# Kernel tuning notes

Hardware: AMD Instinct MI355X
Metric: run time of the kernel (lower is better)

The kernel has to match this reference:

```python
import jax, jax.numpy as jnp
import numpy as np

N_AGENTS = 32
STATE_DIM = 512
EMBED = 64
BATCH = 32768


def setup_inputs() -> dict:
    key = jax.random.key(0)
    ks = jax.random.split(key, 16)
    g = lambda k, shape, fan_in: jax.random.normal(k, shape, jnp.float32) / np.sqrt(fan_in)
    return {
        "agent_qs": jax.random.normal(ks[0], (BATCH, N_AGENTS), jnp.float32),
        "states": jax.random.normal(ks[1], (BATCH, STATE_DIM), jnp.float32),
        # hyper_w1: Linear(state,E) -> ReLU -> Linear(E, n_agents*E)
        "w1_l1_w": g(ks[2], (EMBED, STATE_DIM), STATE_DIM),
        "w1_l1_b": jnp.zeros((EMBED,), jnp.float32),
        "w1_l2_w": g(ks[3], (N_AGENTS * EMBED, EMBED), EMBED),
        "w1_l2_b": jnp.zeros((N_AGENTS * EMBED,), jnp.float32),
        # hyper_w2: Linear(state,E) -> ReLU -> Linear(E, E)
        "w2_l1_w": g(ks[4], (EMBED, STATE_DIM), STATE_DIM),
        "w2_l1_b": jnp.zeros((EMBED,), jnp.float32),
        "w2_l2_w": g(ks[5], (EMBED, EMBED), EMBED),
        "w2_l2_b": jnp.zeros((EMBED,), jnp.float32),
        # hyper_b1: Linear(state, E)
        "b1_w": g(ks[6], (EMBED, STATE_DIM), STATE_DIM),
        "b1_b": jnp.zeros((EMBED,), jnp.float32),
        # hyper_b2: Linear(state,E) -> ReLU -> Linear(E, 1)
        "b2_l1_w": g(ks[7], (EMBED, STATE_DIM), STATE_DIM),
        "b2_l1_b": jnp.zeros((EMBED,), jnp.float32),
        "b2_l2_w": g(ks[8], (1, EMBED), EMBED),
        "b2_l2_b": jnp.zeros((1,), jnp.float32),
    }


def _linear(x, w, b):
    return x @ w.T + b


def reference(agent_qs, states,
              w1_l1_w, w1_l1_b, w1_l2_w, w1_l2_b,
              w2_l1_w, w2_l1_b, w2_l2_w, w2_l2_b,
              b1_w, b1_b, b2_l1_w, b2_l1_b, b2_l2_w, b2_l2_b):
    B = agent_qs.shape[0]
    # hypernetworks producing per-sample weights
    w1 = jnp.abs(_linear(jax.nn.relu(_linear(states, w1_l1_w, w1_l1_b)), w1_l2_w, w1_l2_b))
    w1 = w1.reshape(B, N_AGENTS, EMBED)                      # [B, A, E]
    b1 = _linear(states, b1_w, b1_b)                         # [B, E]
    hidden = jax.nn.elu(jnp.einsum('ba,bae->be', agent_qs, w1) + b1)  # [B, E]
    w2 = jnp.abs(_linear(jax.nn.relu(_linear(states, w2_l1_w, w2_l1_b)), w2_l2_w, w2_l2_b))  # [B, E]
    b2 = _linear(jax.nn.relu(_linear(states, b2_l1_w, b2_l1_b)), b2_l2_w, b2_l2_b)           # [B, 1]
    q_total = jnp.einsum('be,be->b', hidden, w2) + b2[:, 0]  # [B]
    return q_total
```

## Files before the change

kernel.cpp:

```cpp
#include <hip/hip_runtime.h>

typedef unsigned short u16;
typedef unsigned int u32;
typedef short bf16x8 __attribute__((ext_vector_type(8)));
typedef float f32x4 __attribute__((ext_vector_type(4)));
typedef u16 u16x4 __attribute__((ext_vector_type(4)));

#define NAG 32
#define STATE 512
#define EMBED 64
#define TB 64

#define OFF_W1L1 0
#define OFF_W2L1 32768
#define OFF_B1W  65536
#define OFF_B2L1 98304
#define OFF_W1L2 131072
#define OFF_W2L2 262144
#define WS_TOTAL 266240

#define Y_STR    200
#define SB_OFF   12800
#define SB_STR   72
#define SB_BUF   (64 * 72)
#define W1BS_OFF 22016
#define QST_OFF  24064
#define QST_STR  68
#define PBUF_OFF 12800
#define PBUF_STR 68
#define PBUF_WV  (64 * 68)
#define QACC_OFF  30208
#define QACC2_OFF 30336
#define B2WV_OFF  30464
#define SMEM_U16  30592

__device__ __forceinline__ float bf2f(u16 u) {
    u32 i = ((u32)u) << 16; float f;
    __builtin_memcpy(&f, &i, 4); return f;
}
__device__ __forceinline__ u16 f2bf(float f) {
    u32 i; __builtin_memcpy(&i, &f, 4);
    return (u16)((i + 0x8000u) >> 16);
}
__device__ __forceinline__ bf16x8 ld8(const u16* p) {
    return *reinterpret_cast<const bf16x8*>(p);
}
__device__ __forceinline__ bf16x8 cvt8(f32x4 a, f32x4 b) {
    bf16x8 r;
#pragma unroll
    for (int i = 0; i < 4; ++i) r[i]     = (short)f2bf(a[i]);
#pragma unroll
    for (int i = 0; i < 4; ++i) r[i + 4] = (short)f2bf(b[i]);
    return r;
}

__global__ __launch_bounds__(256) void cvt_weights(
    const float* __restrict__ w1l1w, const float* __restrict__ w2l1w,
    const float* __restrict__ b1w,   const float* __restrict__ b2l1w,
    const float* __restrict__ w1l2w, const float* __restrict__ w2l2w,
    u16* __restrict__ ws)
{
    int idx = blockIdx.x * 256 + threadIdx.x;
    const float* src; int off;
    if      (idx < OFF_W2L1)  { src = w1l1w; off = OFF_W1L1; }
    else if (idx < OFF_B1W)   { src = w2l1w; off = OFF_W2L1; }
    else if (idx < OFF_B2L1)  { src = b1w;   off = OFF_B1W;  }
    else if (idx < OFF_W1L2)  { src = b2l1w; off = OFF_B2L1; }
    else if (idx < OFF_W2L2)  { src = w1l2w; off = OFF_W1L2; }
    else if (idx < WS_TOTAL)  { src = w2l2w; off = OFF_W2L2; }
    else return;
    ws[idx] = f2bf(src[idx - off]);
}

__global__ __launch_bounds__(256, 2) void qmix_kernel(
    const float* __restrict__ qs,    const float* __restrict__ st,
    const u16*  __restrict__ wsb,
    const float* __restrict__ w1l1b, const float* __restrict__ w1l2b,
    const float* __restrict__ w2l1b, const float* __restrict__ w2l2b,
    const float* __restrict__ b1b,   const float* __restrict__ b2l1b,
    const float* __restrict__ b2l2w, const float* __restrict__ b2l2b,
    float* __restrict__ out)
{
    __shared__ u16 smem[SMEM_U16];
    float* qaccF  = (float*)(smem + QACC_OFF);
    float* qacc2F = (float*)(smem + QACC2_OFF);
    float* b2wvF  = (float*)(smem + B2WV_OFF);

    const int t    = threadIdx.x;
    const int wave = t >> 6, lane = t & 63;
    const int m = lane & 15, quad = lane >> 4;
    const int sbase = blockIdx.x * TB;

    if (t < 64) b2wvF[t] = b2l2w[t];
    {
        const float* qp = qs + (size_t)sbase * NAG + t * 8;
        f32x4 q0 = *reinterpret_cast<const f32x4*>(qp);
        f32x4 q1 = *reinterpret_cast<const f32x4*>(qp + 4);
        const int s = t >> 2, a0 = (t & 3) * 8;
#pragma unroll
        for (int j = 0; j < 4; ++j) smem[QST_OFF + (a0 + j) * QST_STR + s]     = f2bf(q0[j]);
#pragma unroll
        for (int j = 0; j < 4; ++j) smem[QST_OFF + (a0 + 4 + j) * QST_STR + s] = f2bf(q1[j]);
        f32x4 w0 = *reinterpret_cast<const f32x4*>(w1l2b + t * 8);
        f32x4 w1 = *reinterpret_cast<const f32x4*>(w1l2b + t * 8 + 4);
        *reinterpret_cast<bf16x8*>(&smem[W1BS_OFF + t * 8]) = cvt8(w0, w1);
    }

    const int ss1 = t >> 3, c8 = t & 7;
    const float* stb = st + (size_t)sbase * STATE;

    {
        const float* g1 = stb + (size_t)ss1 * STATE + c8 * 8;
        const float* g2 = g1 + (size_t)32 * STATE;
        f32x4 a0 = *reinterpret_cast<const f32x4*>(g1);
        f32x4 a1 = *reinterpret_cast<const f32x4*>(g1 + 4);
        f32x4 a2 = *reinterpret_cast<const f32x4*>(g2);
        f32x4 a3 = *reinterpret_cast<const f32x4*>(g2 + 4);
        u16* dst = smem + SB_OFF;
        *reinterpret_cast<bf16x8*>(&dst[ss1 * SB_STR + c8 * 8])        = cvt8(a0, a1);
        *reinterpret_cast<bf16x8*>(&dst[(ss1 + 32) * SB_STR + c8 * 8]) = cvt8(a2, a3);
    }

    const u16* wAw = wsb + (size_t)(wave * 64) * STATE;
    bf16x8 bfr[2][4][2];
#pragma unroll
    for (int ot = 0; ot < 4; ++ot) {
        const u16* wr = wAw + (size_t)(ot * 16 + m) * STATE + quad * 8;
        bfr[0][ot][0] = ld8(wr);
        bfr[0][ot][1] = ld8(wr + 32);
    }
    __syncthreads();

    f32x4 acc[4][4] = {};
#pragma unroll
    for (int ks = 0; ks < 8; ++ks) {
        f32x4 sa0 = {}, sa1 = {}, sa2 = {}, sa3 = {};
        if (ks < 7) {
            const float* g1 = stb + (size_t)ss1 * STATE + (ks + 1) * 64 + c8 * 8;
            const float* g2 = g1 + (size_t)32 * STATE;
            sa0 = *reinterpret_cast<const f32x4*>(g1);
            sa1 = *reinterpret_cast<const f32x4*>(g1 + 4);
            sa2 = *reinterpret_cast<const f32x4*>(g2);
            sa3 = *reinterpret_cast<const f32x4*>(g2 + 4);
#pragma unroll
            for (int ot = 0; ot < 4; ++ot) {
                const u16* wr = wAw + (size_t)(ot * 16 + m) * STATE + (ks + 1) * 64 + quad * 8;
                bfr[(ks + 1) & 1][ot][0] = ld8(wr);
                bfr[(ks + 1) & 1][ot][1] = ld8(wr + 32);
            }
        }
        const u16* sbc = smem + SB_OFF + (ks & 1) * SB_BUF;
#pragma unroll
        for (int st2 = 0; st2 < 4; ++st2) {
            const int row = st2 * 16 + m;
            bf16x8 af0 = ld8(&sbc[row * SB_STR + quad * 8]);
            bf16x8 af1 = ld8(&sbc[row * SB_STR + (quad + 4) * 8]);
#pragma unroll
            for (int ot = 0; ot < 4; ++ot)
                acc[st2][ot] = __builtin_amdgcn_mfma_f32_16x16x32_bf16(af0, bfr[ks & 1][ot][0], acc[st2][ot], 0, 0, 0);
#pragma unroll
            for (int ot = 0; ot < 4; ++ot)
                acc[st2][ot] = __builtin_amdgcn_mfma_f32_16x16x32_bf16(af1, bfr[ks & 1][ot][1], acc[st2][ot], 0, 0, 0);
        }
        if (ks < 7) {
            u16* dst = smem + SB_OFF + ((ks + 1) & 1) * SB_BUF;
            *reinterpret_cast<bf16x8*>(&dst[ss1 * SB_STR + c8 * 8])        = cvt8(sa0, sa1);
            *reinterpret_cast<bf16x8*>(&dst[(ss1 + 32) * SB_STR + c8 * 8]) = cvt8(sa2, sa3);
        }
        __syncthreads();
    }

    if (wave != 3) {
        const float* barr = (wave == 0) ? w1l1b : (wave == 1) ? w2l1b : b1b;
        const bool isrelu = (wave != 2);
        float wb[4];
#pragma unroll
        for (int ot = 0; ot < 4; ++ot) wb[ot] = barr[ot * 16 + m];
#pragma unroll
        for (int st2 = 0; st2 < 4; ++st2)
#pragma unroll
            for (int ot = 0; ot < 4; ++ot)
#pragma unroll
                for (int r = 0; r < 4; ++r) {
                    float v = acc[st2][ot][r] + wb[ot];
                    if (isrelu) v = fmaxf(v, 0.f);
                    smem[(st2 * 16 + quad * 4 + r) * Y_STR + wave * 64 + ot * 16 + m] = f2bf(v);
                }
    } else {
        float wb[4], bw[4];
#pragma unroll
        for (int ot = 0; ot < 4; ++ot) wb[ot] = b2l1b[ot * 16 + m];
#pragma unroll
        for (int ot = 0; ot < 4; ++ot) bw[ot] = b2wvF[ot * 16 + m];
#pragma unroll
        for (int st2 = 0; st2 < 4; ++st2)
#pragma unroll
            for (int r = 0; r < 4; ++r) {
                float pd = 0.f;
#pragma unroll
                for (int ot = 0; ot < 4; ++ot)
                    pd += fmaxf(acc[st2][ot][r] + wb[ot], 0.f) * bw[ot];
#pragma unroll
                for (int off = 1; off < 16; off <<= 1) pd += __shfl_xor(pd, off, 64);
                if (m == 0) qacc2F[st2 * 16 + quad * 4 + r] = pd;
            }
    }
    __syncthreads();

    bf16x8 h1f[4][2];
#pragma unroll
    for (int st2 = 0; st2 < 4; ++st2) {
        h1f[st2][0] = ld8(&smem[(st2 * 16 + m) * Y_STR + quad * 8]);
        h1f[st2][1] = ld8(&smem[(st2 * 16 + m) * Y_STR + 32 + quad * 8]);
    }

    const u16* wB = wsb + OFF_W1L2 + (size_t)(wave * 8) * 64 * EMBED;
    bf16x8 bb[2][4][2];
#pragma unroll
    for (int ot = 0; ot < 4; ++ot) {
        const u16* wr = wB + (size_t)(ot * 16 + m) * EMBED + quad * 8;
        bb[0][ot][0] = ld8(wr);
        bb[0][ot][1] = ld8(wr + 32);
    }

    f32x4 hacc[4][4] = {};
#pragma unroll
    for (int ag = 0; ag < 8; ++ag) {
        if (ag < 7) {
#pragma unroll
            for (int ot = 0; ot < 4; ++ot) {
                const u16* wr = wB + (size_t)((ag + 1) * 64 + ot * 16 + m) * EMBED + quad * 8;
                bb[(ag + 1) & 1][ot][0] = ld8(wr);
                bb[(ag + 1) & 1][ot][1] = ld8(wr + 32);
            }
        }
        const int a = wave * 8 + ag;
        float bias[4];
#pragma unroll
        for (int ot = 0; ot < 4; ++ot) bias[ot] = bf2f(smem[W1BS_OFF + a * EMBED + ot * 16 + m]);
#pragma unroll
        for (int st2 = 0; st2 < 4; ++st2) {
            u16x4 qv = *reinterpret_cast<const u16x4*>(&smem[QST_OFF + a * QST_STR + st2 * 16 + quad * 4]);
#pragma unroll
            for (int ot = 0; ot < 4; ++ot) {
                f32x4 p = {};
                p = __builtin_amdgcn_mfma_f32_16x16x32_bf16(h1f[st2][0], bb[ag & 1][ot][0], p, 0, 0, 0);
                p = __builtin_amdgcn_mfma_f32_16x16x32_bf16(h1f[st2][1], bb[ag & 1][ot][1], p, 0, 0, 0);
#pragma unroll
                for (int r = 0; r < 4; ++r)
                    hacc[st2][ot][r] += bf2f((u16)qv[r]) * fabsf(p[r] + bias[ot]);
            }
        }
    }
    __syncthreads();

#pragma unroll
    for (int st2 = 0; st2 < 4; ++st2)
#pragma unroll
        for (int ot = 0; ot < 4; ++ot)
#pragma unroll
            for (int r = 0; r < 4; ++r)
                smem[PBUF_OFF + wave * PBUF_WV + (st2 * 16 + quad * 4 + r) * PBUF_STR + ot * 16 + m]
                    = f2bf(hacc[st2][ot][r]);
    __syncthreads();

    {
        const int s  = wave * 16 + (lane & 15);
        const int eb = (lane >> 4) * 16;
        float v[16];
#pragma unroll
        for (int j = 0; j < 16; ++j) v[j] = 0.f;
#pragma unroll
        for (int pw = 0; pw < 4; ++pw) {
#pragma unroll
            for (int c = 0; c < 4; ++c) {
                u16x4 x = *reinterpret_cast<const u16x4*>(
                    &smem[PBUF_OFF + pw * PBUF_WV + s * PBUF_STR + eb + c * 4]);
#pragma unroll
                for (int j = 0; j < 4; ++j) v[c * 4 + j] += bf2f((u16)x[j]);
            }
        }
        bf16x8 bv0 = ld8(&smem[s * Y_STR + 128 + eb]);
        bf16x8 bv1 = ld8(&smem[s * Y_STR + 128 + eb + 8]);
        bf16x8 o0, o1;
#pragma unroll
        for (int j = 0; j < 8; ++j) {
            float h0 = v[j] + bf2f((u16)bv0[j]);
            h0 = (h0 > 0.f) ? h0 : (__expf(h0) - 1.f);
            o0[j] = (short)f2bf(h0);
            float h1 = v[8 + j] + bf2f((u16)bv1[j]);
            h1 = (h1 > 0.f) ? h1 : (__expf(h1) - 1.f);
            o1[j] = (short)f2bf(h1);
        }
        *reinterpret_cast<bf16x8*>(&smem[s * Y_STR + 128 + eb])     = o0;
        *reinterpret_cast<bf16x8*>(&smem[s * Y_STR + 128 + eb + 8]) = o1;
    }
    __syncthreads();

    const int s0 = wave * 16;
    bf16x8 h2f0 = ld8(&smem[(s0 + m) * Y_STR + 64 + quad * 8]);
    bf16x8 h2f1 = ld8(&smem[(s0 + m) * Y_STR + 96 + quad * 8]);

    f32x4 qp = {};
#pragma unroll
    for (int tp = 0; tp < 4; ++tp) {
        const u16* wc = wsb + OFF_W2L2 + (size_t)(tp * 16 + m) * EMBED + quad * 8;
        bf16x8 c0 = ld8(wc);
        bf16x8 c1 = ld8(wc + 32);
        f32x4 p = {};
        p = __builtin_amdgcn_mfma_f32_16x16x32_bf16(h2f0, c0, p, 0, 0, 0);
        p = __builtin_amdgcn_mfma_f32_16x16x32_bf16(h2f1, c1, p, 0, 0, 0);
        const float bias = w2l2b[tp * 16 + m];
#pragma unroll
        for (int r = 0; r < 4; ++r)
            qp[r] += bf2f(smem[(s0 + quad * 4 + r) * Y_STR + 128 + tp * 16 + m]) * fabsf(p[r] + bias);
    }
#pragma unroll
    for (int off = 1; off < 16; off <<= 1) {
#pragma unroll
        for (int r = 0; r < 4; ++r) qp[r] += __shfl_xor(qp[r], off, 64);
    }
    if (m == 0) {
#pragma unroll
        for (int r = 0; r < 4; ++r) qaccF[s0 + quad * 4 + r] = qp[r];
    }
    __syncthreads();

    if (t < TB) out[sbase + t] = qaccF[t] + qacc2F[t] + b2l2b[0];
}

extern "C" void kernel_launch(void* const* d_in, const int* in_sizes, int n_in,
                              void* d_out, int out_size, void* d_ws, size_t ws_size,
                              hipStream_t stream)
{
    const float* qs    = (const float*)d_in[0];
    const float* st    = (const float*)d_in[1];
    const float* w1l1w = (const float*)d_in[2];
    const float* w1l1b = (const float*)d_in[3];
    const float* w1l2w = (const float*)d_in[4];
    const float* w1l2b = (const float*)d_in[5];
    const float* w2l1w = (const float*)d_in[6];
    const float* w2l1b = (const float*)d_in[7];
    const float* w2l2w = (const float*)d_in[8];
    const float* w2l2b = (const float*)d_in[9];
    const float* b1w   = (const float*)d_in[10];
    const float* b1b   = (const float*)d_in[11];
    const float* b2l1w = (const float*)d_in[12];
    const float* b2l1b = (const float*)d_in[13];
    const float* b2l2w = (const float*)d_in[14];
    const float* b2l2b = (const float*)d_in[15];

    u16* wsb = (u16*)d_ws;

    cvt_weights<<<(WS_TOTAL + 255) / 256, 256, 0, stream>>>(
        w1l1w, w2l1w, b1w, b2l1w, w1l2w, w2l2w, wsb);

    int B = in_sizes[0] / NAG;
    int grid = B / TB;
    qmix_kernel<<<grid, 256, 0, stream>>>(
        qs, st, wsb,
        w1l1b, w1l2b, w2l1b, w2l2b, b1b, b2l1b, b2l2w, b2l2b,
        (float*)d_out);
}
```

Before: 157.3 us.

## Double block to 512 threads and split per-wave work across eight waves

The block now has eight waves instead of four. Each wave takes 32 output columns of the first-layer GEMM, and for the w1 mixing stage the work is split by agent group and sample half. This spreads the same 64-sample tile over more waves, cutting per-thread accumulator registers and raising latency hiding. The launch bound asks for four blocks per CU. The reduction buffer stride is changed to 72, and the b2 partials are split into two halves. The risk is the extra syncthreads cost across 512 threads, half the waves idle in the final stage, and dropping the prefetch double-buffering of the w1l2 weights.

```diff
diff --git a/kernel.cpp b/kernel.cpp
--- a/kernel.cpp
+++ b/kernel.cpp
@@ -27,12 +27,12 @@
 #define QST_OFF  24064
 #define QST_STR  68
 #define PBUF_OFF 12800
-#define PBUF_STR 68
-#define PBUF_WV  (64 * 68)
-#define QACC_OFF  30208
-#define QACC2_OFF 30336
-#define B2WV_OFF  30464
-#define SMEM_U16  30592
+#define PBUF_STR 72
+#define PBUF_WV  (64 * 72)
+#define QACC_OFF  31232
+#define QACC2_OFF 31360
+#define B2WV_OFF  31616
+#define SMEM_U16  31744
 
 __device__ __forceinline__ float bf2f(u16 u) {
     u32 i = ((u32)u) << 16; float f;
@@ -72,7 +72,7 @@
     ws[idx] = f2bf(src[idx - off]);
 }
 
-__global__ __launch_bounds__(256, 2) void qmix_kernel(
+__global__ __launch_bounds__(512, 4) void qmix_kernel(
     const float* __restrict__ qs,    const float* __restrict__ st,
     const u16*  __restrict__ wsb,
     const float* __restrict__ w1l1b, const float* __restrict__ w1l2b,
@@ -92,7 +92,7 @@
     const int sbase = blockIdx.x * TB;
 
     if (t < 64) b2wvF[t] = b2l2w[t];
-    {
+    if (t < 256) {
         const float* qp = qs + (size_t)sbase * NAG + t * 8;
         f32x4 q0 = *reinterpret_cast<const f32x4*>(qp);
         f32x4 q1 = *reinterpret_cast<const f32x4*>(qp + 4);
@@ -101,49 +101,42 @@
         for (int j = 0; j < 4; ++j) smem[QST_OFF + (a0 + j) * QST_STR + s]     = f2bf(q0[j]);
 #pragma unroll
         for (int j = 0; j < 4; ++j) smem[QST_OFF + (a0 + 4 + j) * QST_STR + s] = f2bf(q1[j]);
-        f32x4 w0 = *reinterpret_cast<const f32x4*>(w1l2b + t * 8);
-        f32x4 w1 = *reinterpret_cast<const f32x4*>(w1l2b + t * 8 + 4);
-        *reinterpret_cast<bf16x8*>(&smem[W1BS_OFF + t * 8]) = cvt8(w0, w1);
+    } else {
+        const int i = t & 255;
+        f32x4 w0 = *reinterpret_cast<const f32x4*>(w1l2b + i * 8);
+        f32x4 w1 = *reinterpret_cast<const f32x4*>(w1l2b + i * 8 + 4);
+        *reinterpret_cast<bf16x8*>(&smem[W1BS_OFF + i * 8]) = cvt8(w0, w1);
     }
 
     const int ss1 = t >> 3, c8 = t & 7;
     const float* stb = st + (size_t)sbase * STATE;
-
     {
         const float* g1 = stb + (size_t)ss1 * STATE + c8 * 8;
-        const float* g2 = g1 + (size_t)32 * STATE;
         f32x4 a0 = *reinterpret_cast<const f32x4*>(g1);
         f32x4 a1 = *reinterpret_cast<const f32x4*>(g1 + 4);
-        f32x4 a2 = *reinterpret_cast<const f32x4*>(g2);
-        f32x4 a3 = *reinterpret_cast<const f32x4*>(g2 + 4);
-        u16* dst = smem + SB_OFF;
-        *reinterpret_cast<bf16x8*>(&dst[ss1 * SB_STR + c8 * 8])        = cvt8(a0, a1);
-        *reinterpret_cast<bf16x8*>(&dst[(ss1 + 32) * SB_STR + c8 * 8]) = cvt8(a2, a3);
-    }
-
-    const u16* wAw = wsb + (size_t)(wave * 64) * STATE;
-    bf16x8 bfr[2][4][2];
-#pragma unroll
-    for (int ot = 0; ot < 4; ++ot) {
+        *reinterpret_cast<bf16x8*>(&smem[SB_OFF + ss1 * SB_STR + c8 * 8]) = cvt8(a0, a1);
+    }
+
+    const u16* wAw = wsb + (size_t)(wave * 32) * STATE;
+    bf16x8 bfr[2][2][2];
+#pragma unroll
+    for (int ot = 0; ot < 2; ++ot) {
         const u16* wr = wAw + (size_t)(ot * 16 + m) * STATE + quad * 8;
         bfr[0][ot][0] = ld8(wr);
         bfr[0][ot][1] = ld8(wr + 32);
     }
     __syncthreads();
 
-    f32x4 acc[4][4] = {};
+    f32x4 acc[4][2] = {};
 #pragma unroll
     for (int ks = 0; ks < 8; ++ks) {
-        f32x4 sa0 = {}, sa1 = {}, sa2 = {}, sa3 = {};
+        f32x4 sa0 = {}, sa1 = {};
         if (ks < 7) {
             const float* g1 = stb + (size_t)ss1 * STATE + (ks + 1) * 64 + c8 * 8;
-            const float* g2 = g1 + (size_t)32 * STATE;
             sa0 = *reinterpret_cast<const f32x4*>(g1);
             sa1 = *reinterpret_cast<const f32x4*>(g1 + 4);
-            sa2 = *reinterpret_cast<const f32x4*>(g2);
-            sa3 = *reinterpret_cast<const f32x4*>(g2 + 4);
-#pragma unroll
-            for (int ot = 0; ot < 4; ++ot) {
+#pragma unroll
+            for (int ot = 0; ot < 2; ++ot) {
                 const u16* wr = wAw + (size_t)(ot * 16 + m) * STATE + (ks + 1) * 64 + quad * 8;
                 bfr[(ks + 1) & 1][ot][0] = ld8(wr);
                 bfr[(ks + 1) & 1][ot][1] = ld8(wr + 32);
@@ -156,96 +149,92 @@
             bf16x8 af0 = ld8(&sbc[row * SB_STR + quad * 8]);
             bf16x8 af1 = ld8(&sbc[row * SB_STR + (quad + 4) * 8]);
 #pragma unroll
-            for (int ot = 0; ot < 4; ++ot)
+            for (int ot = 0; ot < 2; ++ot)
                 acc[st2][ot] = __builtin_amdgcn_mfma_f32_16x16x32_bf16(af0, bfr[ks & 1][ot][0], acc[st2][ot], 0, 0, 0);
 #pragma unroll
-            for (int ot = 0; ot < 4; ++ot)
+            for (int ot = 0; ot < 2; ++ot)
                 acc[st2][ot] = __builtin_amdgcn_mfma_f32_16x16x32_bf16(af1, bfr[ks & 1][ot][1], acc[st2][ot], 0, 0, 0);
         }
         if (ks < 7) {
             u16* dst = smem + SB_OFF + ((ks + 1) & 1) * SB_BUF;
-            *reinterpret_cast<bf16x8*>(&dst[ss1 * SB_STR + c8 * 8])        = cvt8(sa0, sa1);
-            *reinterpret_cast<bf16x8*>(&dst[(ss1 + 32) * SB_STR + c8 * 8]) = cvt8(sa2, sa3);
+            *reinterpret_cast<bf16x8*>(&dst[ss1 * SB_STR + c8 * 8]) = cvt8(sa0, sa1);
         }
         __syncthreads();
     }
 
-    if (wave != 3) {
-        const float* barr = (wave == 0) ? w1l1b : (wave == 1) ? w2l1b : b1b;
-        const bool isrelu = (wave != 2);
-        float wb[4];
-#pragma unroll
-        for (int ot = 0; ot < 4; ++ot) wb[ot] = barr[ot * 16 + m];
-#pragma unroll
-        for (int st2 = 0; st2 < 4; ++st2)
-#pragma unroll
-            for (int ot = 0; ot < 4; ++ot)
+    {
+        const int grp = wave >> 1, half = wave & 1;
+        if (grp < 3) {
+            const float* barr = (grp == 0) ? w1l1b : (grp == 1) ? w2l1b : b1b;
+            const bool isrelu = (grp != 2);
+            float wb[2];
+#pragma unroll
+            for (int ot = 0; ot < 2; ++ot) wb[ot] = barr[half * 32 + ot * 16 + m];
+#pragma unroll
+            for (int st2 = 0; st2 < 4; ++st2)
+#pragma unroll
+                for (int ot = 0; ot < 2; ++ot)
+#pragma unroll
+                    for (int r = 0; r < 4; ++r) {
+                        float v = acc[st2][ot][r] + wb[ot];
+                        if (isrelu) v = fmaxf(v, 0.f);
+                        smem[(st2 * 16 + quad * 4 + r) * Y_STR + grp * 64 + half * 32 + ot * 16 + m] = f2bf(v);
+                    }
+        } else {
+            float wb[2], bw[2];
+#pragma unroll
+            for (int ot = 0; ot < 2; ++ot) wb[ot] = b2l1b[half * 32 + ot * 16 + m];
+#pragma unroll
+            for (int ot = 0; ot < 2; ++ot) bw[ot] = b2wvF[half * 32 + ot * 16 + m];
+#pragma unroll
+            for (int st2 = 0; st2 < 4; ++st2)
 #pragma unroll
                 for (int r = 0; r < 4; ++r) {
-                    float v = acc[st2][ot][r] + wb[ot];
-                    if (isrelu) v = fmaxf(v, 0.f);
-                    smem[(st2 * 16 + quad * 4 + r) * Y_STR + wave * 64 + ot * 16 + m] = f2bf(v);
+                    float pd = 0.f;
+#pragma unroll
+                    for (int ot = 0; ot < 2; ++ot)
+                        pd += fmaxf(acc[st2][ot][r] + wb[ot], 0.f) * bw[ot];
+#pragma unroll
+                    for (int off = 1; off < 16; off <<= 1) pd += __shfl_xor(pd, off, 64);
+                    if (m == 0) qacc2F[half * 64 + st2 * 16 + quad * 4 + r] = pd;
                 }
-    } else {
-        float wb[4], bw[4];
-#pragma unroll
-        for (int ot = 0; ot < 4; ++ot) wb[ot] = b2l1b[ot * 16 + m];
-#pragma unroll
-        for (int ot = 0; ot < 4; ++ot) bw[ot] = b2wvF[ot * 16 + m];
-#pragma unroll
-        for (int st2 = 0; st2 < 4; ++st2)
-#pragma unroll
-            for (int r = 0; r < 4; ++r) {
-                float pd = 0.f;
-#pragma unroll
-                for (int ot = 0; ot < 4; ++ot)
-                    pd += fmaxf(acc[st2][ot][r] + wb[ot], 0.f) * bw[ot];
-#pragma unroll
-                for (int off = 1; off < 16; off <<= 1) pd += __shfl_xor(pd, off, 64);
-                if (m == 0) qacc2F[st2 * 16 + quad * 4 + r] = pd;
-            }
-    }
-    __syncthreads();
-
-    bf16x8 h1f[4][2];
-#pragma unroll
-    for (int st2 = 0; st2 < 4; ++st2) {
-        h1f[st2][0] = ld8(&smem[(st2 * 16 + m) * Y_STR + quad * 8]);
-        h1f[st2][1] = ld8(&smem[(st2 * 16 + m) * Y_STR + 32 + quad * 8]);
-    }
-
-    const u16* wB = wsb + OFF_W1L2 + (size_t)(wave * 8) * 64 * EMBED;
-    bf16x8 bb[2][4][2];
-#pragma unroll
-    for (int ot = 0; ot < 4; ++ot) {
-        const u16* wr = wB + (size_t)(ot * 16 + m) * EMBED + quad * 8;
-        bb[0][ot][0] = ld8(wr);
-        bb[0][ot][1] = ld8(wr + 32);
-    }
-
-    f32x4 hacc[4][4] = {};
+        }
+    }
+    __syncthreads();
+
+    const int ah = wave & 3, sh = wave >> 2;
+    bf16x8 h1f[2][2];
+#pragma unroll
+    for (int st2 = 0; st2 < 2; ++st2) {
+        const int row = sh * 32 + st2 * 16 + m;
+        h1f[st2][0] = ld8(&smem[row * Y_STR + quad * 8]);
+        h1f[st2][1] = ld8(&smem[row * Y_STR + 32 + quad * 8]);
+    }
+
+    const u16* wB = wsb + OFF_W1L2 + (size_t)(ah * 8) * 64 * EMBED;
+    f32x4 hacc[2][4] = {};
 #pragma unroll
     for (int ag = 0; ag < 8; ++ag) {
-        if (ag < 7) {
-#pragma unroll
-            for (int ot = 0; ot < 4; ++ot) {
-                const u16* wr = wB + (size_t)((ag + 1) * 64 + ot * 16 + m) * EMBED + quad * 8;
-                bb[(ag + 1) & 1][ot][0] = ld8(wr);
-                bb[(ag + 1) & 1][ot][1] = ld8(wr + 32);
-            }
-        }
-        const int a = wave * 8 + ag;
+        const int a = ah * 8 + ag;
+        bf16x8 bb[4][2];
+#pragma unroll
+        for (int ot = 0; ot < 4; ++ot) {
+            const u16* wr = wB + (size_t)(ag * 64 + ot * 16 + m) * EMBED + quad * 8;
+            bb[ot][0] = ld8(wr);
+            bb[ot][1] = ld8(wr + 32);
+        }
         float bias[4];
 #pragma unroll
         for (int ot = 0; ot < 4; ++ot) bias[ot] = bf2f(smem[W1BS_OFF + a * EMBED + ot * 16 + m]);
 #pragma unroll
-        for (int st2 = 0; st2 < 4; ++st2) {
-            u16x4 qv = *reinterpret_cast<const u16x4*>(&smem[QST_OFF + a * QST_STR + st2 * 16 + quad * 4]);
+        for (int st2 = 0; st2 < 2; ++st2) {
+            u16x4 qv = *reinterpret_cast<const u16x4*>(
+                &smem[QST_OFF + a * QST_STR + sh * 32 + st2 * 16 + quad * 4]);
 #pragma unroll
             for (int ot = 0; ot < 4; ++ot) {
                 f32x4 p = {};
-                p = __builtin_amdgcn_mfma_f32_16x16x32_bf16(h1f[st2][0], bb[ag & 1][ot][0], p, 0, 0, 0);
-                p = __builtin_amdgcn_mfma_f32_16x16x32_bf16(h1f[st2][1], bb[ag & 1][ot][1], p, 0, 0, 0);
+                p = __builtin_amdgcn_mfma_f32_16x16x32_bf16(h1f[st2][0], bb[ot][0], p, 0, 0, 0);
+                p = __builtin_amdgcn_mfma_f32_16x16x32_bf16(h1f[st2][1], bb[ot][1], p, 0, 0, 0);
 #pragma unroll
                 for (int r = 0; r < 4; ++r)
                     hacc[st2][ot][r] += bf2f((u16)qv[r]) * fabsf(p[r] + bias[ot]);
@@ -255,78 +244,77 @@
     __syncthreads();
 
 #pragma unroll
-    for (int st2 = 0; st2 < 4; ++st2)
+    for (int st2 = 0; st2 < 2; ++st2)
 #pragma unroll
         for (int ot = 0; ot < 4; ++ot)
 #pragma unroll
             for (int r = 0; r < 4; ++r)
-                smem[PBUF_OFF + wave * PBUF_WV + (st2 * 16 + quad * 4 + r) * PBUF_STR + ot * 16 + m]
+                smem[PBUF_OFF + ah * PBUF_WV
+                     + (sh * 32 + st2 * 16 + quad * 4 + r) * PBUF_STR + ot * 16 + m]
                     = f2bf(hacc[st2][ot][r]);
     __syncthreads();
 
     {
-        const int s  = wave * 16 + (lane & 15);
-        const int eb = (lane >> 4) * 16;
-        float v[16];
-#pragma unroll
-        for (int j = 0; j < 16; ++j) v[j] = 0.f;
+        const int s  = t >> 3;
+        const int eb = (t & 7) * 8;
+        float v[8];
+#pragma unroll
+        for (int j = 0; j < 8; ++j) v[j] = 0.f;
 #pragma unroll
         for (int pw = 0; pw < 4; ++pw) {
-#pragma unroll
-            for (int c = 0; c < 4; ++c) {
-                u16x4 x = *reinterpret_cast<const u16x4*>(
-                    &smem[PBUF_OFF + pw * PBUF_WV + s * PBUF_STR + eb + c * 4]);
-#pragma unroll
-                for (int j = 0; j < 4; ++j) v[c * 4 + j] += bf2f((u16)x[j]);
-            }
-        }
-        bf16x8 bv0 = ld8(&smem[s * Y_STR + 128 + eb]);
-        bf16x8 bv1 = ld8(&smem[s * Y_STR + 128 + eb + 8]);
-        bf16x8 o0, o1;
+            u16x4 x0 = *reinterpret_cast<const u16x4*>(
+                &smem[PBUF_OFF + pw * PBUF_WV + s * PBUF_STR + eb]);
+            u16x4 x1 = *reinterpret_cast<const u16x4*>(
+                &smem[PBUF_OFF + pw * PBUF_WV + s * PBUF_STR + eb + 4]);
+#pragma unroll
+            for (int j = 0; j < 4; ++j) v[j]     += bf2f((u16)x0[j]);
+#pragma unroll
+            for (int j = 0; j < 4; ++j) v[4 + j] += bf2f((u16)x1[j]);
+        }
+        bf16x8 bv = ld8(&smem[s * Y_STR + 128 + eb]);
+        bf16x8 o;
 #pragma unroll
         for (int j = 0; j < 8; ++j) {
-            float h0 = v[j] + bf2f((u16)bv0[j]);
-            h0 = (h0 > 0.f) ? h0 : (__expf(h0) - 1.f);
-            o0[j] = (short)f2bf(h0);
-            float h1 = v[8 + j] + bf2f((u16)bv1[j]);
-            h1 = (h1 > 0.f) ? h1 : (__expf(h1) - 1.f);
-            o1[j] = (short)f2bf(h1);
-        }
-        *reinterpret_cast<bf16x8*>(&smem[s * Y_STR + 128 + eb])     = o0;
-        *reinterpret_cast<bf16x8*>(&smem[s * Y_STR + 128 + eb + 8]) = o1;
-    }
-    __syncthreads();
-
-    const int s0 = wave * 16;
-    bf16x8 h2f0 = ld8(&smem[(s0 + m) * Y_STR + 64 + quad * 8]);
-    bf16x8 h2f1 = ld8(&smem[(s0 + m) * Y_STR + 96 + quad * 8]);
-
-    f32x4 qp = {};
-#pragma unroll
-    for (int tp = 0; tp < 4; ++tp) {
-        const u16* wc = wsb + OFF_W2L2 + (size_t)(tp * 16 + m) * EMBED + quad * 8;
-        bf16x8 c0 = ld8(wc);
-        bf16x8 c1 = ld8(wc + 32);
-        f32x4 p = {};
-        p = __builtin_amdgcn_mfma_f32_16x16x32_bf16(h2f0, c0, p, 0, 0, 0);
-        p = __builtin_amdgcn_mfma_f32_16x16x32_bf16(h2f1, c1, p, 0, 0, 0);
-        const float bias = w2l2b[tp * 16 + m];
-#pragma unroll
-        for (int r = 0; r < 4; ++r)
-            qp[r] += bf2f(smem[(s0 + quad * 4 + r) * Y_STR + 128 + tp * 16 + m]) * fabsf(p[r] + bias);
-    }
-#pragma unroll
-    for (int off = 1; off < 16; off <<= 1) {
-#pragma unroll
-        for (int r = 0; r < 4; ++r) qp[r] += __shfl_xor(qp[r], off, 64);
-    }
-    if (m == 0) {
-#pragma unroll
-        for (int r = 0; r < 4; ++r) qaccF[s0 + quad * 4 + r] = qp[r];
-    }
-    __syncthreads();
-
-    if (t < TB) out[sbase + t] = qaccF[t] + qacc2F[t] + b2l2b[0];
+            float h = v[j] + bf2f((u16)bv[j]);
+            h = (h > 0.f) ? h : (__expf(h) - 1.f);
+            o[j] = (short)f2bf(h);
+        }
+        *reinterpret_cast<bf16x8*>(&smem[s * Y_STR + 128 + eb]) = o;
+    }
+    __syncthreads();
+
+    if (wave < 4) {
+        const int s0 = wave * 16;
+        bf16x8 h2f0 = ld8(&smem[(s0 + m) * Y_STR + 64 + quad * 8]);
+        bf16x8 h2f1 = ld8(&smem[(s0 + m) * Y_STR + 96 + quad * 8]);
+
+        f32x4 qp = {};
+#pragma unroll
+        for (int tp = 0; tp < 4; ++tp) {
+            const u16* wc = wsb + OFF_W2L2 + (size_t)(tp * 16 + m) * EMBED + quad * 8;
+            bf16x8 c0 = ld8(wc);
+            bf16x8 c1 = ld8(wc + 32);
+            f32x4 p = {};
+            p = __builtin_amdgcn_mfma_f32_16x16x32_bf16(h2f0, c0, p, 0, 0, 0);
+            p = __builtin_amdgcn_mfma_f32_16x16x32_bf16(h2f1, c1, p, 0, 0, 0);
+            const float bias = w2l2b[tp * 16 + m];
+#pragma unroll
+            for (int r = 0; r < 4; ++r)
+                qp[r] += bf2f(smem[(s0 + quad * 4 + r) * Y_STR + 128 + tp * 16 + m]) * fabsf(p[r] + bias);
+        }
+#pragma unroll
+        for (int off = 1; off < 16; off <<= 1) {
+#pragma unroll
+            for (int r = 0; r < 4; ++r) qp[r] += __shfl_xor(qp[r], off, 64);
+        }
+        if (m == 0) {
+#pragma unroll
+            for (int r = 0; r < 4; ++r) qaccF[s0 + quad * 4 + r] = qp[r];
+        }
+    }
+    __syncthreads();
+
+    if (t < TB) out[sbase + t] = qaccF[t] + qacc2F[t] + qacc2F[64 + t] + b2l2b[0];
 }
 
 extern "C" void kernel_launch(void* const* d_in, const int* in_sizes, int n_in,
@@ -357,7 +345,7 @@
 
     int B = in_sizes[0] / NAG;
     int grid = B / TB;
-    qmix_kernel<<<grid, 256, 0, stream>>>(
+    qmix_kernel<<<grid, 512, 0, stream>>>(
         qs, st, wsb,
         w1l1b, w1l2b, w2l1b, w2l2b, b1b, b2l1b, b2l2w, b2l2b,
         (float*)d_out);
```

Result: slower. 168.5 us (+7.2%).

## Stage weight tiles into LDS via global_load_lds DMA with XOR swizzle

Applied to the files above, without the earlier changes.

Replaces the per-lane register prefetch of the layer-1 and W1-layer-2 weight fragments with direct global-to-LDS DMA (global_load_lds) into an XOR-swizzled shared buffer. MFMA operands are then read from LDS. The double-buffered state staging and register prefetch pipeline are removed, so each k-step now does a load, a full waitcnt(0) and two barriers before compute. This lowers register pressure and VGPR traffic but serialises loads and compute, and it grows the LDS footprint, which may reduce occupancy.

```diff
diff --git a/kernel.cpp b/kernel.cpp
--- a/kernel.cpp
+++ b/kernel.cpp
@@ -19,20 +19,21 @@
 #define OFF_W2L2 262144
 #define WS_TOTAL 266240
 
+#define WBUF_OFF 0
+#define SB_OFF   16384
+#define SB_STR   72
+#define QST_OFF  20992
+#define QST_STR  68
+#define W1BS_OFF 23168
+#define Y_OFF    25216
 #define Y_STR    200
-#define SB_OFF   12800
-#define SB_STR   72
-#define SB_BUF   (64 * 72)
-#define W1BS_OFF 22016
-#define QST_OFF  24064
-#define QST_STR  68
-#define PBUF_OFF 12800
-#define PBUF_STR 68
-#define PBUF_WV  (64 * 68)
-#define QACC_OFF  30208
-#define QACC2_OFF 30336
-#define B2WV_OFF  30464
-#define SMEM_U16  30592
+#define PBUF_OFF 0
+#define PBUF_STR 72
+#define PBUF_WV  (64 * 72)
+#define QACC_OFF  38016
+#define QACC2_OFF 38144
+#define B2WV_OFF  38272
+#define SMEM_U16  38400
 
 __device__ __forceinline__ float bf2f(u16 u) {
     u32 i = ((u32)u) << 16; float f;
@@ -52,6 +53,11 @@
 #pragma unroll
     for (int i = 0; i < 4; ++i) r[i + 4] = (short)f2bf(b[i]);
     return r;
+}
+__device__ __forceinline__ void dma16(const void* g, void* l) {
+    __builtin_amdgcn_global_load_lds(
+        (const __attribute__((address_space(1))) u32*)g,
+        (__attribute__((address_space(3))) u32*)l, 16, 0, 0);
 }
 
 __global__ __launch_bounds__(256) void cvt_weights(
@@ -89,6 +95,8 @@
     const int t    = threadIdx.x;
     const int wave = t >> 6, lane = t & 63;
     const int m = lane & 15, quad = lane >> 4;
+    const int rsub = lane >> 3, cch = lane & 7;
+    const int sc = cch ^ rsub;
     const int sbase = blockIdx.x * TB;
 
     if (t < 64) b2wvF[t] = b2l2w[t];
@@ -109,68 +117,47 @@
     const int ss1 = t >> 3, c8 = t & 7;
     const float* stb = st + (size_t)sbase * STATE;
 
-    {
-        const float* g1 = stb + (size_t)ss1 * STATE + c8 * 8;
-        const float* g2 = g1 + (size_t)32 * STATE;
-        f32x4 a0 = *reinterpret_cast<const f32x4*>(g1);
-        f32x4 a1 = *reinterpret_cast<const f32x4*>(g1 + 4);
-        f32x4 a2 = *reinterpret_cast<const f32x4*>(g2);
-        f32x4 a3 = *reinterpret_cast<const f32x4*>(g2 + 4);
-        u16* dst = smem + SB_OFF;
-        *reinterpret_cast<bf16x8*>(&dst[ss1 * SB_STR + c8 * 8])        = cvt8(a0, a1);
-        *reinterpret_cast<bf16x8*>(&dst[(ss1 + 32) * SB_STR + c8 * 8]) = cvt8(a2, a3);
-    }
-
-    const u16* wAw = wsb + (size_t)(wave * 64) * STATE;
-    bf16x8 bfr[2][4][2];
-#pragma unroll
-    for (int ot = 0; ot < 4; ++ot) {
-        const u16* wr = wAw + (size_t)(ot * 16 + m) * STATE + quad * 8;
-        bfr[0][ot][0] = ld8(wr);
-        bfr[0][ot][1] = ld8(wr + 32);
-    }
-    __syncthreads();
-
     f32x4 acc[4][4] = {};
-#pragma unroll
     for (int ks = 0; ks < 8; ++ks) {
-        f32x4 sa0 = {}, sa1 = {}, sa2 = {}, sa3 = {};
-        if (ks < 7) {
-            const float* g1 = stb + (size_t)ss1 * STATE + (ks + 1) * 64 + c8 * 8;
+        __syncthreads();
+#pragma unroll
+        for (int j = 0; j < 8; ++j)
+            dma16(wsb + (size_t)(wave * 64 + j * 8 + rsub) * STATE + ks * 64 + sc * 8,
+                  &smem[WBUF_OFF + (wave * 64 + j * 8) * 64]);
+        {
+            const float* g1 = stb + (size_t)ss1 * STATE + ks * 64 + c8 * 8;
             const float* g2 = g1 + (size_t)32 * STATE;
-            sa0 = *reinterpret_cast<const f32x4*>(g1);
-            sa1 = *reinterpret_cast<const f32x4*>(g1 + 4);
-            sa2 = *reinterpret_cast<const f32x4*>(g2);
-            sa3 = *reinterpret_cast<const f32x4*>(g2 + 4);
-#pragma unroll
-            for (int ot = 0; ot < 4; ++ot) {
-                const u16* wr = wAw + (size_t)(ot * 16 + m) * STATE + (ks + 1) * 64 + quad * 8;
-                bfr[(ks + 1) & 1][ot][0] = ld8(wr);
-                bfr[(ks + 1) & 1][ot][1] = ld8(wr + 32);
-            }
-        }
-        const u16* sbc = smem + SB_OFF + (ks & 1) * SB_BUF;
+            f32x4 a0 = *reinterpret_cast<const f32x4*>(g1);
+            f32x4 a1 = *reinterpret_cast<const f32x4*>(g1 + 4);
+            f32x4 a2 = *reinterpret_cast<const f32x4*>(g2);
+            f32x4 a3 = *reinterpret_cast<const f32x4*>(g2 + 4);
+            *reinterpret_cast<bf16x8*>(&smem[SB_OFF + ss1 * SB_STR + c8 * 8])        = cvt8(a0, a1);
+            *reinterpret_cast<bf16x8*>(&smem[SB_OFF + (ss1 + 32) * SB_STR + c8 * 8]) = cvt8(a2, a3);
+        }
+        __builtin_amdgcn_s_waitcnt(0);
+        __syncthreads();
+        bf16x8 wfr[4][2];
+#pragma unroll
+        for (int ot = 0; ot < 4; ++ot) {
+            const int brow = wave * 64 + ot * 16 + m;
+            wfr[ot][0] = ld8(&smem[WBUF_OFF + brow * 64 + ((quad ^ (brow & 7))) * 8]);
+            wfr[ot][1] = ld8(&smem[WBUF_OFF + brow * 64 + (((quad + 4) ^ (brow & 7))) * 8]);
+        }
 #pragma unroll
         for (int st2 = 0; st2 < 4; ++st2) {
             const int row = st2 * 16 + m;
-            bf16x8 af0 = ld8(&sbc[row * SB_STR + quad * 8]);
-            bf16x8 af1 = ld8(&sbc[row * SB_STR + (quad + 4) * 8]);
+            bf16x8 af0 = ld8(&smem[SB_OFF + row * SB_STR + quad * 8]);
+            bf16x8 af1 = ld8(&smem[SB_OFF + row * SB_STR + (quad + 4) * 8]);
 #pragma unroll
             for (int ot = 0; ot < 4; ++ot)
-                acc[st2][ot] = __builtin_amdgcn_mfma_f32_16x16x32_bf16(af0, bfr[ks & 1][ot][0], acc[st2][ot], 0, 0, 0);
+                acc[st2][ot] = __builtin_amdgcn_mfma_f32_16x16x32_bf16(af0, wfr[ot][0], acc[st2][ot], 0, 0, 0);
 #pragma unroll
             for (int ot = 0; ot < 4; ++ot)
-                acc[st2][ot] = __builtin_amdgcn_mfma_f32_16x16x32_bf16(af1, bfr[ks & 1][ot][1], acc[st2][ot], 0, 0, 0);
-        }
-        if (ks < 7) {
-            u16* dst = smem + SB_OFF + ((ks + 1) & 1) * SB_BUF;
-            *reinterpret_cast<bf16x8*>(&dst[ss1 * SB_STR + c8 * 8])        = cvt8(sa0, sa1);
-            *reinterpret_cast<bf16x8*>(&dst[(ss1 + 32) * SB_STR + c8 * 8]) = cvt8(sa2, sa3);
-        }
-        __syncthreads();
-    }
-
-    if (wave != 3) {
+                acc[st2][ot] = __builtin_amdgcn_mfma_f32_16x16x32_bf16(af1, wfr[ot][1], acc[st2][ot], 0, 0, 0);
+        }
+    }
+
+    if (wave < 3) {
         const float* barr = (wave == 0) ? w1l1b : (wave == 1) ? w2l1b : b1b;
         const bool isrelu = (wave != 2);
         float wb[4];
@@ -184,7 +171,7 @@
                 for (int r = 0; r < 4; ++r) {
                     float v = acc[st2][ot][r] + wb[ot];
                     if (isrelu) v = fmaxf(v, 0.f);
-                    smem[(st2 * 16 + quad * 4 + r) * Y_STR + wave * 64 + ot * 16 + m] = f2bf(v);
+                    smem[Y_OFF + (st2 * 16 + quad * 4 + r) * Y_STR + wave * 64 + ot * 16 + m] = f2bf(v);
                 }
     } else {
         float wb[4], bw[4];
@@ -210,58 +197,56 @@
     bf16x8 h1f[4][2];
 #pragma unroll
     for (int st2 = 0; st2 < 4; ++st2) {
-        h1f[st2][0] = ld8(&smem[(st2 * 16 + m) * Y_STR + quad * 8]);
-        h1f[st2][1] = ld8(&smem[(st2 * 16 + m) * Y_STR + 32 + quad * 8]);
-    }
-
-    const u16* wB = wsb + OFF_W1L2 + (size_t)(wave * 8) * 64 * EMBED;
-    bf16x8 bb[2][4][2];
-#pragma unroll
-    for (int ot = 0; ot < 4; ++ot) {
-        const u16* wr = wB + (size_t)(ot * 16 + m) * EMBED + quad * 8;
-        bb[0][ot][0] = ld8(wr);
-        bb[0][ot][1] = ld8(wr + 32);
+        h1f[st2][0] = ld8(&smem[Y_OFF + (st2 * 16 + m) * Y_STR + quad * 8]);
+        h1f[st2][1] = ld8(&smem[Y_OFF + (st2 * 16 + m) * Y_STR + 32 + quad * 8]);
     }
 
     f32x4 hacc[4][4] = {};
-#pragma unroll
-    for (int ag = 0; ag < 8; ++ag) {
-        if (ag < 7) {
-#pragma unroll
-            for (int ot = 0; ot < 4; ++ot) {
-                const u16* wr = wB + (size_t)((ag + 1) * 64 + ot * 16 + m) * EMBED + quad * 8;
-                bb[(ag + 1) & 1][ot][0] = ld8(wr);
-                bb[(ag + 1) & 1][ot][1] = ld8(wr + 32);
+    for (int j = 0; j < 8; ++j) {
+        __syncthreads();
+        const int a = wave * 8 + j;
+#pragma unroll
+        for (int jj = 0; jj < 8; ++jj)
+            dma16(wsb + OFF_W1L2 + (size_t)(a * 64 + jj * 8 + rsub) * EMBED + sc * 8,
+                  &smem[WBUF_OFF + (wave * 64 + jj * 8) * 64]);
+        __builtin_amdgcn_s_waitcnt(0);
+        __syncthreads();
+        bf16x8 wf[4][2];
+#pragma unroll
+        for (int tp = 0; tp < 4; ++tp) {
+            const int brow = wave * 64 + tp * 16 + m;
+            wf[tp][0] = ld8(&smem[WBUF_OFF + brow * 64 + ((quad ^ (brow & 7))) * 8]);
+            wf[tp][1] = ld8(&smem[WBUF_OFF + brow * 64 + (((quad + 4) ^ (brow & 7))) * 8]);
+        }
+        float bias[4];
+#pragma unroll
+        for (int tp = 0; tp < 4; ++tp) bias[tp] = bf2f(smem[W1BS_OFF + a * EMBED + tp * 16 + m]);
+#pragma unroll
+        for (int st2 = 0; st2 < 4; ++st2) {
+            u16x4 qv = *reinterpret_cast<const u16x4*>(
+                &smem[QST_OFF + a * QST_STR + st2 * 16 + quad * 4]);
+#pragma unroll
+            for (int tp = 0; tp < 4; ++tp) {
+                f32x4 p = {};
+                p = __builtin_amdgcn_mfma_f32_16x16x32_bf16(h1f[st2][0], wf[tp][0], p, 0, 0, 0);
+                p = __builtin_amdgcn_mfma_f32_16x16x32_bf16(h1f[st2][1], wf[tp][1], p, 0, 0, 0);
+#pragma unroll
+                for (int r = 0; r < 4; ++r)
+                    hacc[st2][tp][r] += bf2f((u16)qv[r]) * fabsf(p[r] + bias[tp]);
             }
         }
-        const int a = wave * 8 + ag;
-        float bias[4];
-#pragma unroll
-        for (int ot = 0; ot < 4; ++ot) bias[ot] = bf2f(smem[W1BS_OFF + a * EMBED + ot * 16 + m]);
-#pragma unroll
-        for (int st2 = 0; st2 < 4; ++st2) {
-            u16x4 qv = *reinterpret_cast<const u16x4*>(&smem[QST_OFF + a * QST_STR + st2 * 16 + quad * 4]);
-#pragma unroll
-            for (int ot = 0; ot < 4; ++ot) {
-                f32x4 p = {};
-                p = __builtin_amdgcn_mfma_f32_16x16x32_bf16(h1f[st2][0], bb[ag & 1][ot][0], p, 0, 0, 0);
-                p = __builtin_amdgcn_mfma_f32_16x16x32_bf16(h1f[st2][1], bb[ag & 1][ot][1], p, 0, 0, 0);
-#pragma unroll
-                for (int r = 0; r < 4; ++r)
-                    hacc[st2][ot][r] += bf2f((u16)qv[r]) * fabsf(p[r] + bias[ot]);
-            }
-        }
     }
     __syncthreads();
 
 #pragma unroll
     for (int st2 = 0; st2 < 4; ++st2)
 #pragma unroll
-        for (int ot = 0; ot < 4; ++ot)
+        for (int tp = 0; tp < 4; ++tp)
 #pragma unroll
             for (int r = 0; r < 4; ++r)
-                smem[PBUF_OFF + wave * PBUF_WV + (st2 * 16 + quad * 4 + r) * PBUF_STR + ot * 16 + m]
-                    = f2bf(hacc[st2][ot][r]);
+                smem[PBUF_OFF + wave * PBUF_WV
+                     + (st2 * 16 + quad * 4 + r) * PBUF_STR + tp * 16 + m]
+                    = f2bf(hacc[st2][tp][r]);
     __syncthreads();
 
     {
@@ -269,7 +254,7 @@
         const int eb = (lane >> 4) * 16;
         float v[16];
 #pragma unroll
-        for (int j = 0; j < 16; ++j) v[j] = 0.f;
+        for (int jj = 0; jj < 16; ++jj) v[jj] = 0.f;
 #pragma unroll
         for (int pw = 0; pw < 4; ++pw) {
 #pragma unroll
@@ -277,52 +262,55 @@
                 u16x4 x = *reinterpret_cast<const u16x4*>(
                     &smem[PBUF_OFF + pw * PBUF_WV + s * PBUF_STR + eb + c * 4]);
 #pragma unroll
-                for (int j = 0; j < 4; ++j) v[c * 4 + j] += bf2f((u16)x[j]);
+                for (int jj = 0; jj < 4; ++jj) v[c * 4 + jj] += bf2f((u16)x[jj]);
             }
         }
-        bf16x8 bv0 = ld8(&smem[s * Y_STR + 128 + eb]);
-        bf16x8 bv1 = ld8(&smem[s * Y_STR + 128 + eb + 8]);
+        bf16x8 bv0 = ld8(&smem[Y_OFF + s * Y_STR + 128 + eb]);
+        bf16x8 bv1 = ld8(&smem[Y_OFF + s * Y_STR + 128 + eb + 8]);
         bf16x8 o0, o1;
 #pragma unroll
-        for (int j = 0; j < 8; ++j) {
-            float h0 = v[j] + bf2f((u16)bv0[j]);
+        for (int jj = 0; jj < 8; ++jj) {
+            float h0 = v[jj] + bf2f((u16)bv0[jj]);
             h0 = (h0 > 0.f) ? h0 : (__expf(h0) - 1.f);
-            o0[j] = (short)f2bf(h0);
-            float h1 = v[8 + j] + bf2f((u16)bv1[j]);
+            o0[jj] = (short)f2bf(h0);
+            float h1 = v[8 + jj] + bf2f((u16)bv1[jj]);
             h1 = (h1 > 0.f) ? h1 : (__expf(h1) - 1.f);
-            o1[j] = (short)f2bf(h1);
-        }
-        *reinterpret_cast<bf16x8*>(&smem[s * Y_STR + 128 + eb])     = o0;
-        *reinterpret_cast<bf16x8*>(&smem[s * Y_STR + 128 + eb + 8]) = o1;
-    }
-    __syncthreads();
-
-    const int s0 = wave * 16;
-    bf16x8 h2f0 = ld8(&smem[(s0 + m) * Y_STR + 64 + quad * 8]);
-    bf16x8 h2f1 = ld8(&smem[(s0 + m) * Y_STR + 96 + quad * 8]);
-
-    f32x4 qp = {};
-#pragma unroll
-    for (int tp = 0; tp < 4; ++tp) {
-        const u16* wc = wsb + OFF_W2L2 + (size_t)(tp * 16 + m) * EMBED + quad * 8;
-        bf16x8 c0 = ld8(wc);
-        bf16x8 c1 = ld8(wc + 32);
-        f32x4 p = {};
-        p = __builtin_amdgcn_mfma_f32_16x16x32_bf16(h2f0, c0, p, 0, 0, 0);
-        p = __builtin_amdgcn_mfma_f32_16x16x32_bf16(h2f1, c1, p, 0, 0, 0);
-        const float bias = w2l2b[tp * 16 + m];
-#pragma unroll
-        for (int r = 0; r < 4; ++r)
-            qp[r] += bf2f(smem[(s0 + quad * 4 + r) * Y_STR + 128 + tp * 16 + m]) * fabsf(p[r] + bias);
-    }
-#pragma unroll
-    for (int off = 1; off < 16; off <<= 1) {
-#pragma unroll
-        for (int r = 0; r < 4; ++r) qp[r] += __shfl_xor(qp[r], off, 64);
-    }
-    if (m == 0) {
-#pragma unroll
-        for (int r = 0; r < 4; ++r) qaccF[s0 + quad * 4 + r] = qp[r];
+            o1[jj] = (short)f2bf(h1);
+        }
+        *reinterpret_cast<bf16x8*>(&smem[Y_OFF + s * Y_STR + 128 + eb])     = o0;
+        *reinterpret_cast<bf16x8*>(&smem[Y_OFF + s * Y_STR + 128 + eb + 8]) = o1;
+    }
+    __syncthreads();
+
+    {
+        const int s0 = wave * 16;
+        bf16x8 h2f0 = ld8(&smem[Y_OFF + (s0 + m) * Y_STR + 64 + quad * 8]);
+        bf16x8 h2f1 = ld8(&smem[Y_OFF + (s0 + m) * Y_STR + 96 + quad * 8]);
+
+        f32x4 qp = {};
+#pragma unroll
+        for (int tp = 0; tp < 4; ++tp) {
+            const u16* wc = wsb + OFF_W2L2 + (size_t)(tp * 16 + m) * EMBED + quad * 8;
+            bf16x8 c0 = ld8(wc);
+            bf16x8 c1 = ld8(wc + 32);
+            f32x4 p = {};
+            p = __builtin_amdgcn_mfma_f32_16x16x32_bf16(h2f0, c0, p, 0, 0, 0);
+            p = __builtin_amdgcn_mfma_f32_16x16x32_bf16(h2f1, c1, p, 0, 0, 0);
+            const float bias = w2l2b[tp * 16 + m];
+#pragma unroll
+            for (int r = 0; r < 4; ++r)
+                qp[r] += bf2f(smem[Y_OFF + (s0 + quad * 4 + r) * Y_STR + 128 + tp * 16 + m])
+                         * fabsf(p[r] + bias);
+        }
+#pragma unroll
+        for (int off = 1; off < 16; off <<= 1) {
+#pragma unroll
+            for (int r = 0; r < 4; ++r) qp[r] += __shfl_xor(qp[r], off, 64);
+        }
+        if (m == 0) {
+#pragma unroll
+            for (int r = 0; r < 4; ++r) qaccF[s0 + quad * 4 + r] = qp[r];
+        }
     }
     __syncthreads();
 
```

After: 147.5 us. 1.07x faster.
